# Kernel tuning notes

Measured on AMD Instinct MI355X. Metric: run time of the kernel, lower is better.

The kernel has to match this reference:

```python
import jax, jax.numpy as jnp
import numpy as np

N = 100000   # nodes
E = 1000000  # directed edges
C = 64       # channels
K = 4        # propagation hops
DT = 1.0     # dt; exp_init=False branch: 2*x + dt^2*conv(x) - x_pre


def setup_inputs() -> dict:
    key = jax.random.key(0)
    k1, k2, k3, k4, k5 = jax.random.split(key, 5)
    x = jax.random.normal(k1, (N, C), dtype=jnp.float32)
    x_pre = jax.random.normal(k2, (N, C), dtype=jnp.float32)
    edge_index = jax.random.randint(k3, (2, E), 0, N, dtype=jnp.int32)
    bound = 1.0 / np.sqrt(C)  # PyG Linear default (kaiming-uniform-like)
    W = jax.random.uniform(k4, (C, C), jnp.float32, -bound, bound)
    b = jax.random.uniform(k5, (C,), jnp.float32, -bound, bound)
    return {"x": x, "x_pre": x_pre, "edge_index": edge_index, "W": W, "b": b}


def _sgc(x, edge_index, W, b):
    # gcn_norm: add self-loops, symmetric normalization D^-1/2 (A+I) D^-1/2
    loop = jnp.arange(N, dtype=edge_index.dtype)
    src = jnp.concatenate([edge_index[0], loop])  # source j
    dst = jnp.concatenate([edge_index[1], loop])  # target i
    deg = jax.ops.segment_sum(jnp.ones(src.shape, jnp.float32), dst, num_segments=N)
    dinv = jnp.where(deg > 0, jax.lax.rsqrt(deg), 0.0)
    norm = dinv[src] * dinv[dst]  # [E+N]
    h = x
    for _ in range(K):  # K-hop sparse propagation (gather -> scale -> scatter-add)
        h = jax.ops.segment_sum(h[src] * norm[:, None], dst, num_segments=N)
    return h @ W.T + b  # SGConv final linear


def reference(x, x_pre, edge_index, W, b):
    return 2.0 * x + (DT * DT) * _sgc(x, edge_index, W, b) - x_pre
```

## Files before the change

### kernel.cpp

```cpp
#include <hip/hip_runtime.h>
#include <hip/hip_fp16.h>

#define CCH 64
#define NBLK 128
#define BKT  256


__global__ void countA(const int* __restrict__ dst, int* __restrict__ cntmat,
                       int E, int chunk, int B) {
    __shared__ int h[512];
    int t = threadIdx.x, blk = blockIdx.x;
    for (int i = t; i < B; i += 256) h[i] = 0;
    __syncthreads();
    int e0 = blk * chunk, e1 = min(e0 + chunk, E);
    for (int e = e0 + t; e < e1; e += 256) atomicAdd(&h[dst[e] >> 8], 1);
    __syncthreads();
    for (int i = t; i < B; i += 256) cntmat[i * NBLK + blk] = h[i];
}

__global__ void scan1(const int* __restrict__ cnt, int* __restrict__ part,
                      int* __restrict__ bsum, int N) {
    __shared__ int s[256];
    int t = threadIdx.x;
    int base = blockIdx.x * 1024 + t * 4;
    int v0 = (base + 0 < N) ? cnt[base + 0] : 0;
    int v1 = (base + 1 < N) ? cnt[base + 1] : 0;
    int v2 = (base + 2 < N) ? cnt[base + 2] : 0;
    int v3 = (base + 3 < N) ? cnt[base + 3] : 0;
    s[t] = v0 + v1 + v2 + v3;
    __syncthreads();
    for (int off = 1; off < 256; off <<= 1) {
        int xx = (t >= off) ? s[t - off] : 0;
        __syncthreads();
        s[t] += xx;
        __syncthreads();
    }
    int excl = (t == 0) ? 0 : s[t - 1];
    if (t == 255) bsum[blockIdx.x] = s[255];
    if (base + 0 < N) part[base + 0] = excl;
    if (base + 1 < N) part[base + 1] = excl + v0;
    if (base + 2 < N) part[base + 2] = excl + v0 + v1;
    if (base + 3 < N) part[base + 3] = excl + v0 + v1 + v2;
}

__device__ __forceinline__ void scan_bsum(const int* __restrict__ bsum, int NB2,
                                          int* sbs, int t) {
    int v = (t < NB2) ? bsum[t] : 0;
    sbs[t] = v;
    __syncthreads();
    for (int o = 1; o < 256; o <<= 1) {
        int xx = (t >= o) ? sbs[t - o] : 0;
        __syncthreads();
        sbs[t] += xx;
        __syncthreads();
    }
    int e = sbs[t] - v;
    __syncthreads();
    sbs[t] = e;
    __syncthreads();
}

__global__ void partA(const int* __restrict__ src, const int* __restrict__ dst,
                      const int* __restrict__ part, const int* __restrict__ bsum,
                      unsigned* __restrict__ brec, int E, int chunk, int B, int NB2) {
    __shared__ int cur[512];
    __shared__ int sbs[256];
    int t = threadIdx.x, blk = blockIdx.x;
    scan_bsum(bsum, NB2, sbs, t);
    for (int i = t; i < B; i += 256) {
        int idx = i * NBLK + blk;
        cur[i] = part[idx] + sbs[idx >> 10];
    }
    __syncthreads();
    int e0 = blk * chunk, e1 = min(e0 + chunk, E);
    for (int e = e0 + t; e < e1; e += 256) {
        int s = src[e], d = dst[e];
        int pos = atomicAdd(&cur[d >> 8], 1);
        brec[pos] = ((unsigned)s << 8) | (unsigned)(d & 255);
    }
}

__global__ void buildB(const unsigned* __restrict__ brec, const int* __restrict__ part,
                       const int* __restrict__ bsum, int* __restrict__ row_ptr,
                       int* __restrict__ adj, float* __restrict__ dinv,
                       float* __restrict__ dinv2, const float* __restrict__ x,
                       __half* __restrict__ xh, int N, int B, int E, int NB2) {
    __shared__ int hist[256];
    __shared__ int scanbuf[256];
    __shared__ int cursor[256];
    __shared__ int sbs[256];
    __shared__ float sdinv[256];
    int t = threadIdx.x, k = blockIdx.x;
    scan_bsum(bsum, NB2, sbs, t);
    int i0 = k * NBLK;
    int base = part[i0] + sbs[i0 >> 10];
    int nextb;
    if (k + 1 < B) {
        int i1 = (k + 1) * NBLK;
        nextb = part[i1] + sbs[i1 >> 10];
    } else {
        nextb = E;
    }
    hist[t] = 0;
    __syncthreads();
    for (int i = base + t; i < nextb; i += 256) atomicAdd(&hist[brec[i] & 255u], 1);
    __syncthreads();
    int v = hist[t];
    scanbuf[t] = v;
    __syncthreads();
    for (int o = 1; o < 256; o <<= 1) {
        int xx = (t >= o) ? scanbuf[t - o] : 0;
        __syncthreads();
        scanbuf[t] += xx;
        __syncthreads();
    }
    int excl = scanbuf[t] - v;
    int node = k * 256 + t;
    float di = 0.f;
    if (node < N) {
        int p = base + excl;
        row_ptr[node] = p;
        cursor[t] = p;
        float dp1 = (float)v + 1.0f;
        di = rsqrtf(dp1);
        dinv[node]  = di;
        dinv2[node] = 1.0f / dp1;
    }
    sdinv[t] = di;
    if (k == 0 && t == 0) row_ptr[N] = E;
    __syncthreads();
    for (int i = base + t; i < nextb; i += 256) {
        unsigned r = brec[i];
        int pos = atomicAdd(&cursor[r & 255u], 1);
        adj[pos] = (int)(r >> 8);
    }
    int nodeBase = k * 256;
    for (int i = t; i < 2048; i += 256) {
        int nl = i >> 3;
        int node2 = nodeBase + nl;
        if (node2 < N) {
            float d = sdinv[nl];
            size_t baseE = (size_t)node2 * 64 + (size_t)(i & 7) * 8;
            float4 a = *(const float4*)&x[baseE];
            float4 c = *(const float4*)&x[baseE + 4];
            float4 o;
            __half2* op = (__half2*)&o;
            op[0] = __float22half2_rn(make_float2(d * a.x, d * a.y));
            op[1] = __float22half2_rn(make_float2(d * a.z, d * a.w));
            op[2] = __float22half2_rn(make_float2(d * c.x, d * c.y));
            op[3] = __float22half2_rn(make_float2(d * c.z, d * c.w));
            *(float4*)&xh[baseE] = o;
        }
    }
}


__device__ __forceinline__ void acc16w(float4 hv, float w, float* acc) {
    __half2* hp = (__half2*)&hv;
    #pragma unroll
    for (int i2 = 0; i2 < 4; ++i2) {
        float2 f = __half22float2(hp[i2]);
        acc[2 * i2]     = fmaf(w, f.x, acc[2 * i2]);
        acc[2 * i2 + 1] = fmaf(w, f.y, acc[2 * i2 + 1]);
    }
}

__device__ __forceinline__ void prop_body(const __half* __restrict__ hin,
                                          const int* __restrict__ row_ptr,
                                          const int* __restrict__ adj,
                                          int nodeC, int cnt, int g8, int q,
                                          int E, float* acc) {
    int rp0 = row_ptr[nodeC];

    int R = cnt;
    R = max(R, __shfl_xor(R, 8, 64));
    R = max(R, __shfl_xor(R, 16, 64));
    R = max(R, __shfl_xor(R, 32, 64));

    const float4* hin16 = (const float4*)hin;
    float4 selfv = hin16[(size_t)nodeC * 8 + q];

    int eCur = adj[rp0 + q];
    int eNxt = adj[rp0 + 8 + q];
    int j0 = __shfl(eCur, g8 + 0, 64); j0 = (0 < cnt) ? j0 : 0;
    int j1 = __shfl(eCur, g8 + 1, 64); j1 = (1 < cnt) ? j1 : 0;
    int j2 = __shfl(eCur, g8 + 2, 64); j2 = (2 < cnt) ? j2 : 0;
    int j3 = __shfl(eCur, g8 + 3, 64); j3 = (3 < cnt) ? j3 : 0;
    float4 gA0 = hin16[(size_t)j0 * 8 + q];
    float4 gA1 = hin16[(size_t)j1 * 8 + q];
    float4 gA2 = hin16[(size_t)j2 * 8 + q];
    float4 gA3 = hin16[(size_t)j3 * 8 + q];
    float4 gB0, gB1, gB2, gB3;

    acc16w(selfv, 1.f, acc);

    for (int r = 0; r < R; r += 8) {
        int t;
        t = r + 4; j0 = __shfl(eCur, g8 + (t & 7), 64); j0 = (t < cnt) ? j0 : 0;
        t = r + 5; j1 = __shfl(eCur, g8 + (t & 7), 64); j1 = (t < cnt) ? j1 : 0;
        t = r + 6; j2 = __shfl(eCur, g8 + (t & 7), 64); j2 = (t < cnt) ? j2 : 0;
        t = r + 7; j3 = __shfl(eCur, g8 + (t & 7), 64); j3 = (t < cnt) ? j3 : 0;
        gB0 = hin16[(size_t)j0 * 8 + q];
        gB1 = hin16[(size_t)j1 * 8 + q];
        gB2 = hin16[(size_t)j2 * 8 + q];
        gB3 = hin16[(size_t)j3 * 8 + q];
        float w;
        w = (r + 0 < cnt) ? 1.f : 0.f; acc16w(gA0, w, acc);
        w = (r + 1 < cnt) ? 1.f : 0.f; acc16w(gA1, w, acc);
        w = (r + 2 < cnt) ? 1.f : 0.f; acc16w(gA2, w, acc);
        w = (r + 3 < cnt) ? 1.f : 0.f; acc16w(gA3, w, acc);
        t = r + 8;  j0 = __shfl(eNxt, g8 + (t & 7), 64); j0 = (t < cnt) ? j0 : 0;
        t = r + 9;  j1 = __shfl(eNxt, g8 + (t & 7), 64); j1 = (t < cnt) ? j1 : 0;
        t = r + 10; j2 = __shfl(eNxt, g8 + (t & 7), 64); j2 = (t < cnt) ? j2 : 0;
        t = r + 11; j3 = __shfl(eNxt, g8 + (t & 7), 64); j3 = (t < cnt) ? j3 : 0;
        gA0 = hin16[(size_t)j0 * 8 + q];
        gA1 = hin16[(size_t)j1 * 8 + q];
        gA2 = hin16[(size_t)j2 * 8 + q];
        gA3 = hin16[(size_t)j3 * 8 + q];
        w = (r + 4 < cnt) ? 1.f : 0.f; acc16w(gB0, w, acc);
        w = (r + 5 < cnt) ? 1.f : 0.f; acc16w(gB1, w, acc);
        w = (r + 6 < cnt) ? 1.f : 0.f; acc16w(gB2, w, acc);
        w = (r + 7 < cnt) ? 1.f : 0.f; acc16w(gB3, w, acc);
        eCur = eNxt;
        int ao = rp0 + r + 16;
        ao = (ao > E + 96) ? (E + 96) : ao;
        eNxt = adj[ao + q];
    }
}

__global__ void __launch_bounds__(256, 8)
prop_kernel(const __half* __restrict__ hin, __half* __restrict__ hout,
            const int* __restrict__ row_ptr, const int* __restrict__ adj,
            const float* __restrict__ scale, int N, int E) {
    int wid  = (blockIdx.x * blockDim.x + threadIdx.x) >> 6;
    int lane = threadIdx.x & 63;
    int g    = lane >> 3;
    int q    = lane & 7;
    int nb   = wid << 3;
    if (nb >= N) return;
    int  node  = nb + g;
    bool valid = node < N;
    int  nodeC = valid ? node : (N - 1);
    int cnt = valid ? (row_ptr[nodeC + 1] - row_ptr[nodeC]) : 0;

    float acc[8] = {0.f, 0.f, 0.f, 0.f, 0.f, 0.f, 0.f, 0.f};
    prop_body(hin, row_ptr, adj, nodeC, cnt, g << 3, q, E, acc);

    if (valid) {
        float sc = scale[nodeC];
        float4 o;
        __half2* op = (__half2*)&o;
        op[0] = __float22half2_rn(make_float2(sc * acc[0], sc * acc[1]));
        op[1] = __float22half2_rn(make_float2(sc * acc[2], sc * acc[3]));
        op[2] = __float22half2_rn(make_float2(sc * acc[4], sc * acc[5]));
        op[3] = __float22half2_rn(make_float2(sc * acc[6], sc * acc[7]));
        ((float4*)hout)[(size_t)node * 8 + q] = o;
    }
}

__global__ void __launch_bounds__(256, 6)
prop_final_kernel(const __half* __restrict__ hin, const float* __restrict__ x,
                  const float* __restrict__ xp, const float* __restrict__ W,
                  const float* __restrict__ b, float* __restrict__ out,
                  const int* __restrict__ row_ptr, const int* __restrict__ adj,
                  const float* __restrict__ dinv, int N, int E) {
    __shared__ __align__(16) float Wt[64 * 68];
    __shared__ __align__(16) float ht[32 * 68];
    int t = threadIdx.x;
    int nodeBase = blockIdx.x * 32;

    for (int i = t; i < 1024; i += 256) {
        int c  = i >> 4;
        int k4 = i & 15;
        float4 w4 = ((const float4*)W)[i];
        Wt[(k4 * 4 + 0) * 68 + c] = w4.x;
        Wt[(k4 * 4 + 1) * 68 + c] = w4.y;
        Wt[(k4 * 4 + 2) * 68 + c] = w4.z;
        Wt[(k4 * 4 + 3) * 68 + c] = w4.w;
    }

    int wv   = t >> 6;
    int lane = t & 63;
    int g    = lane >> 3;
    int q    = lane & 7;
    int nl   = wv * 8 + g;
    int node = nodeBase + nl;
    bool valid = node < N;
    int  nodeC = valid ? node : (N - 1);
    int cnt = valid ? (row_ptr[nodeC + 1] - row_ptr[nodeC]) : 0;

    float acc[8] = {0.f, 0.f, 0.f, 0.f, 0.f, 0.f, 0.f, 0.f};
    prop_body(hin, row_ptr, adj, nodeC, cnt, g << 3, q, E, acc);

    float sc = valid ? dinv[nodeC] : 0.f;
    {
        float* hrow = &ht[nl * 68 + q * 8];
        float4 h0, h1;
        h0.x = sc * acc[0]; h0.y = sc * acc[1]; h0.z = sc * acc[2]; h0.w = sc * acc[3];
        h1.x = sc * acc[4]; h1.y = sc * acc[5]; h1.z = sc * acc[6]; h1.w = sc * acc[7];
        *(float4*)&hrow[0] = h0;
        *(float4*)&hrow[4] = h1;
    }

    int r0 = t >> 4;
    int c0 = (t & 15) * 4;
    int n0 = nodeBase + r0;
    int n1 = n0 + 16;
    int n0c = (n0 < N) ? n0 : (N - 1);
    int n1c = (n1 < N) ? n1 : (N - 1);
    float4 xv0 = *(const float4*)&x[n0c * 64 + c0];
    float4 pv0 = *(const float4*)&xp[n0c * 64 + c0];
    float4 xv1 = *(const float4*)&x[n1c * 64 + c0];
    float4 pv1 = *(const float4*)&xp[n1c * 64 + c0];
    float4 bv  = *(const float4*)&b[c0];

    __syncthreads();

    float4 av0 = make_float4(0.f, 0.f, 0.f, 0.f);
    float4 av1 = make_float4(0.f, 0.f, 0.f, 0.f);
    #pragma unroll 4
    for (int k4 = 0; k4 < 16; ++k4) {
        float4 w0 = *(const float4*)&Wt[(k4 * 4 + 0) * 68 + c0];
        float4 w1 = *(const float4*)&Wt[(k4 * 4 + 1) * 68 + c0];
        float4 w2 = *(const float4*)&Wt[(k4 * 4 + 2) * 68 + c0];
        float4 w3 = *(const float4*)&Wt[(k4 * 4 + 3) * 68 + c0];
        float4 ha = *(const float4*)&ht[r0 * 68 + k4 * 4];
        float4 hb = *(const float4*)&ht[(r0 + 16) * 68 + k4 * 4];
        av0.x = fmaf(ha.x, w0.x, av0.x); av0.y = fmaf(ha.x, w0.y, av0.y);
        av0.z = fmaf(ha.x, w0.z, av0.z); av0.w = fmaf(ha.x, w0.w, av0.w);
        av0.x = fmaf(ha.y, w1.x, av0.x); av0.y = fmaf(ha.y, w1.y, av0.y);
        av0.z = fmaf(ha.y, w1.z, av0.z); av0.w = fmaf(ha.y, w1.w, av0.w);
        av0.x = fmaf(ha.z, w2.x, av0.x); av0.y = fmaf(ha.z, w2.y, av0.y);
        av0.z = fmaf(ha.z, w2.z, av0.z); av0.w = fmaf(ha.z, w2.w, av0.w);
        av0.x = fmaf(ha.w, w3.x, av0.x); av0.y = fmaf(ha.w, w3.y, av0.y);
        av0.z = fmaf(ha.w, w3.z, av0.z); av0.w = fmaf(ha.w, w3.w, av0.w);
        av1.x = fmaf(hb.x, w0.x, av1.x); av1.y = fmaf(hb.x, w0.y, av1.y);
        av1.z = fmaf(hb.x, w0.z, av1.z); av1.w = fmaf(hb.x, w0.w, av1.w);
        av1.x = fmaf(hb.y, w1.x, av1.x); av1.y = fmaf(hb.y, w1.y, av1.y);
        av1.z = fmaf(hb.y, w1.z, av1.z); av1.w = fmaf(hb.y, w1.w, av1.w);
        av1.x = fmaf(hb.z, w2.x, av1.x); av1.y = fmaf(hb.z, w2.y, av1.y);
        av1.z = fmaf(hb.z, w2.z, av1.z); av1.w = fmaf(hb.z, w2.w, av1.w);
        av1.x = fmaf(hb.w, w3.x, av1.x); av1.y = fmaf(hb.w, w3.y, av1.y);
        av1.z = fmaf(hb.w, w3.z, av1.z); av1.w = fmaf(hb.w, w3.w, av1.w);
    }

    if (n0 < N) {
        int base = n0 * 64 + c0;
        float4 o;
        o.x = fmaf(2.f, xv0.x, av0.x + bv.x) - pv0.x;
        o.y = fmaf(2.f, xv0.y, av0.y + bv.y) - pv0.y;
        o.z = fmaf(2.f, xv0.z, av0.z + bv.z) - pv0.z;
        o.w = fmaf(2.f, xv0.w, av0.w + bv.w) - pv0.w;
        *(float4*)&out[base] = o;
    }
    if (n1 < N) {
        int base = n1 * 64 + c0;
        float4 o;
        o.x = fmaf(2.f, xv1.x, av1.x + bv.x) - pv1.x;
        o.y = fmaf(2.f, xv1.y, av1.y + bv.y) - pv1.y;
        o.z = fmaf(2.f, xv1.z, av1.z + bv.z) - pv1.z;
        o.w = fmaf(2.f, xv1.w, av1.w + bv.w) - pv1.w;
        *(float4*)&out[base] = o;
    }
}

extern "C" void kernel_launch(void* const* d_in, const int* in_sizes, int n_in,
                              void* d_out, int out_size, void* d_ws, size_t ws_size,
                              hipStream_t stream) {
    const float* x    = (const float*)d_in[0];
    const float* xpre = (const float*)d_in[1];
    const int*   ei   = (const int*)d_in[2];
    const float* W    = (const float*)d_in[3];
    const float* b    = (const float*)d_in[4];
    float* out = (float*)d_out;

    const int N = in_sizes[0] / CCH;
    const int E = in_sizes[2] / 2;
    const int* src = ei;
    const int* dst = ei + E;

    const int B     = (N + BKT - 1) / BKT;
    const int M     = B * NBLK;
    const int chunk = (E + NBLK - 1) / NBLK;
    const int NB2   = (M + 1023) / 1024;

    char* p = (char*)d_ws;
    auto alloc = [&](size_t bytes) -> char* {
        char* r = p;
        p += (bytes + 255) & ~(size_t)255;
        return r;
    };
    int*      cntmat  = (int*)alloc((size_t)M * 4);
    int*      part    = (int*)alloc((size_t)M * 4);
    int*      bsum    = (int*)alloc((size_t)NB2 * 4);
    unsigned* brec    = (unsigned*)alloc((size_t)E * 4);
    int*      adj     = (int*)alloc(((size_t)E + 128) * 4);
    int*      row_ptr = (int*)alloc(((size_t)N + 1) * 4);
    float*    dinv    = (float*)alloc((size_t)N * 4);
    float*    dinv2   = (float*)alloc((size_t)N * 4);
    __half*   xh      = (__half*)alloc((size_t)N * CCH * 2);
    __half*   g0      = (__half*)alloc((size_t)N * CCH * 2);
    __half*   g1      = (__half*)alloc((size_t)N * CCH * 2);

    countA<<<NBLK, 256, 0, stream>>>(dst, cntmat, E, chunk, B);
    scan1 <<<NB2, 256, 0, stream>>>(cntmat, part, bsum, M);
    partA <<<NBLK, 256, 0, stream>>>(src, dst, part, bsum, brec, E, chunk, B, NB2);
    buildB<<<B, 256, 0, stream>>>(brec, part, bsum, row_ptr, adj, dinv, dinv2,
                                  x, xh, N, B, E, NB2);

    const int nwave = (N + 7) / 8;
    const int pgrid = (nwave + 3) / 4;
    prop_kernel<<<pgrid, 256, 0, stream>>>(xh, g0, row_ptr, adj, dinv2, N, E);
    prop_kernel<<<pgrid, 256, 0, stream>>>(g0, g1, row_ptr, adj, dinv2, N, E);
    prop_kernel<<<pgrid, 256, 0, stream>>>(g1, g0, row_ptr, adj, dinv2, N, E);
    prop_final_kernel<<<(N + 31) / 32, 256, 0, stream>>>(g0, x, xpre, W, b, out,
                                                         row_ptr, adj, dinv, N, E);
    (void)g1;
}
```

Measured before the change: 245.1 us.

## Sort nodes by degree within buckets to balance per-wave gather work

buildB now counting-sorts the nodes of each 256-node bucket by in-degree and writes a permutation array. All propagation kernels index nodes through this permutation, so the eight nodes sharing a wave have similar degree and less lane divergence in the unrolled gather loop. The final kernel also loads W into shared memory with scalar transposed reads instead of float4 scatter. The cost is an extra indirection per node, a few more scans in buildB, and scattered output rows instead of contiguous ones.

```diff
diff --git a/kernel.cpp b/kernel.cpp
--- a/kernel.cpp
+++ b/kernel.cpp
@@ -84,11 +84,13 @@
                        const int* __restrict__ bsum, int* __restrict__ row_ptr,
                        int* __restrict__ adj, float* __restrict__ dinv,
                        float* __restrict__ dinv2, const float* __restrict__ x,
-                       __half* __restrict__ xh, int N, int B, int E, int NB2) {
+                       __half* __restrict__ xh, int* __restrict__ perm,
+                       int N, int B, int E, int NB2) {
     __shared__ int hist[256];
     __shared__ int scanbuf[256];
     __shared__ int cursor[256];
     __shared__ int sbs[256];
+    __shared__ int dh[256];
     __shared__ float sdinv[256];
     int t = threadIdx.x, k = blockIdx.x;
     scan_bsum(bsum, NB2, sbs, t);
@@ -102,6 +104,7 @@
         nextb = E;
     }
     hist[t] = 0;
+    dh[t] = 0;
     __syncthreads();
     for (int i = base + t; i < nextb; i += 256) atomicAdd(&hist[brec[i] & 255u], 1);
     __syncthreads();
@@ -117,6 +120,7 @@
     int excl = scanbuf[t] - v;
     int node = k * 256 + t;
     float di = 0.f;
+    int d = 255;
     if (node < N) {
         int p = base + excl;
         row_ptr[node] = p;
@@ -125,30 +129,48 @@
         di = rsqrtf(dp1);
         dinv[node]  = di;
         dinv2[node] = 1.0f / dp1;
+        d = (v < 255) ? v : 254;
     }
     sdinv[t] = di;
     if (k == 0 && t == 0) row_ptr[N] = E;
+    atomicAdd(&dh[d], 1);
     __syncthreads();
     for (int i = base + t; i < nextb; i += 256) {
         unsigned r = brec[i];
         int pos = atomicAdd(&cursor[r & 255u], 1);
         adj[pos] = (int)(r >> 8);
+    }
+    __syncthreads();
+    int dv = dh[t];
+    scanbuf[t] = dv;
+    __syncthreads();
+    for (int o = 1; o < 256; o <<= 1) {
+        int xx = (t >= o) ? scanbuf[t - o] : 0;
+        __syncthreads();
+        scanbuf[t] += xx;
+        __syncthreads();
+    }
+    hist[t] = scanbuf[t] - dv;
+    __syncthreads();
+    if (node < N) {
+        int r = atomicAdd(&hist[d], 1);
+        perm[k * 256 + r] = node;
     }
     int nodeBase = k * 256;
     for (int i = t; i < 2048; i += 256) {
         int nl = i >> 3;
         int node2 = nodeBase + nl;
         if (node2 < N) {
-            float d = sdinv[nl];
+            float dsc = sdinv[nl];
             size_t baseE = (size_t)node2 * 64 + (size_t)(i & 7) * 8;
             float4 a = *(const float4*)&x[baseE];
             float4 c = *(const float4*)&x[baseE + 4];
             float4 o;
             __half2* op = (__half2*)&o;
-            op[0] = __float22half2_rn(make_float2(d * a.x, d * a.y));
-            op[1] = __float22half2_rn(make_float2(d * a.z, d * a.w));
-            op[2] = __float22half2_rn(make_float2(d * c.x, d * c.y));
-            op[3] = __float22half2_rn(make_float2(d * c.z, d * c.w));
+            op[0] = __float22half2_rn(make_float2(dsc * a.x, dsc * a.y));
+            op[1] = __float22half2_rn(make_float2(dsc * a.z, dsc * a.w));
+            op[2] = __float22half2_rn(make_float2(dsc * c.x, dsc * c.y));
+            op[3] = __float22half2_rn(make_float2(dsc * c.z, dsc * c.w));
             *(float4*)&xh[baseE] = o;
         }
     }
@@ -231,23 +253,24 @@
 __global__ void __launch_bounds__(256, 8)
 prop_kernel(const __half* __restrict__ hin, __half* __restrict__ hout,
             const int* __restrict__ row_ptr, const int* __restrict__ adj,
-            const float* __restrict__ scale, int N, int E) {
+            const float* __restrict__ scale, const int* __restrict__ perm,
+            int N, int E) {
     int wid  = (blockIdx.x * blockDim.x + threadIdx.x) >> 6;
     int lane = threadIdx.x & 63;
     int g    = lane >> 3;
     int q    = lane & 7;
     int nb   = wid << 3;
     if (nb >= N) return;
-    int  node  = nb + g;
-    bool valid = node < N;
-    int  nodeC = valid ? node : (N - 1);
-    int cnt = valid ? (row_ptr[nodeC + 1] - row_ptr[nodeC]) : 0;
+    int  slot  = nb + g;
+    bool valid = slot < N;
+    int  node  = perm[valid ? slot : (N - 1)];
+    int cnt = valid ? (row_ptr[node + 1] - row_ptr[node]) : 0;
 
     float acc[8] = {0.f, 0.f, 0.f, 0.f, 0.f, 0.f, 0.f, 0.f};
-    prop_body(hin, row_ptr, adj, nodeC, cnt, g << 3, q, E, acc);
+    prop_body(hin, row_ptr, adj, node, cnt, g << 3, q, E, acc);
 
     if (valid) {
-        float sc = scale[nodeC];
+        float sc = scale[node];
         float4 o;
         __half2* op = (__half2*)&o;
         op[0] = __float22half2_rn(make_float2(sc * acc[0], sc * acc[1]));
@@ -263,20 +286,21 @@
                   const float* __restrict__ xp, const float* __restrict__ W,
                   const float* __restrict__ b, float* __restrict__ out,
                   const int* __restrict__ row_ptr, const int* __restrict__ adj,
-                  const float* __restrict__ dinv, int N, int E) {
+                  const float* __restrict__ dinv, const int* __restrict__ perm,
+                  int N, int E) {
     __shared__ __align__(16) float Wt[64 * 68];
     __shared__ __align__(16) float ht[32 * 68];
     int t = threadIdx.x;
     int nodeBase = blockIdx.x * 32;
 
-    for (int i = t; i < 1024; i += 256) {
-        int c  = i >> 4;
-        int k4 = i & 15;
-        float4 w4 = ((const float4*)W)[i];
-        Wt[(k4 * 4 + 0) * 68 + c] = w4.x;
-        Wt[(k4 * 4 + 1) * 68 + c] = w4.y;
-        Wt[(k4 * 4 + 2) * 68 + c] = w4.z;
-        Wt[(k4 * 4 + 3) * 68 + c] = w4.w;
+    {
+        int kr = t >> 6;
+        int c  = t & 63;
+        #pragma unroll
+        for (int it = 0; it < 16; ++it) {
+            int kk = it * 4 + kr;
+            Wt[kk * 68 + c] = W[c * 64 + kk];
+        }
     }
 
     int wv   = t >> 6;
@@ -284,15 +308,15 @@
     int g    = lane >> 3;
     int q    = lane & 7;
     int nl   = wv * 8 + g;
-    int node = nodeBase + nl;
-    bool valid = node < N;
-    int  nodeC = valid ? node : (N - 1);
-    int cnt = valid ? (row_ptr[nodeC + 1] - row_ptr[nodeC]) : 0;
+    int slot = nodeBase + nl;
+    bool valid = slot < N;
+    int  node  = perm[valid ? slot : (N - 1)];
+    int cnt = valid ? (row_ptr[node + 1] - row_ptr[node]) : 0;
 
     float acc[8] = {0.f, 0.f, 0.f, 0.f, 0.f, 0.f, 0.f, 0.f};
-    prop_body(hin, row_ptr, adj, nodeC, cnt, g << 3, q, E, acc);
-
-    float sc = valid ? dinv[nodeC] : 0.f;
+    prop_body(hin, row_ptr, adj, node, cnt, g << 3, q, E, acc);
+
+    float sc = valid ? dinv[node] : 0.f;
     {
         float* hrow = &ht[nl * 68 + q * 8];
         float4 h0, h1;
@@ -304,14 +328,14 @@
 
     int r0 = t >> 4;
     int c0 = (t & 15) * 4;
-    int n0 = nodeBase + r0;
-    int n1 = n0 + 16;
-    int n0c = (n0 < N) ? n0 : (N - 1);
-    int n1c = (n1 < N) ? n1 : (N - 1);
-    float4 xv0 = *(const float4*)&x[n0c * 64 + c0];
-    float4 pv0 = *(const float4*)&xp[n0c * 64 + c0];
-    float4 xv1 = *(const float4*)&x[n1c * 64 + c0];
-    float4 pv1 = *(const float4*)&xp[n1c * 64 + c0];
+    int s0 = nodeBase + r0;
+    int s1 = s0 + 16;
+    int n0 = perm[(s0 < N) ? s0 : (N - 1)];
+    int n1 = perm[(s1 < N) ? s1 : (N - 1)];
+    float4 xv0 = *(const float4*)&x[n0 * 64 + c0];
+    float4 pv0 = *(const float4*)&xp[n0 * 64 + c0];
+    float4 xv1 = *(const float4*)&x[n1 * 64 + c0];
+    float4 pv1 = *(const float4*)&xp[n1 * 64 + c0];
     float4 bv  = *(const float4*)&b[c0];
 
     __syncthreads();
@@ -344,7 +368,7 @@
         av1.z = fmaf(hb.w, w3.z, av1.z); av1.w = fmaf(hb.w, w3.w, av1.w);
     }
 
-    if (n0 < N) {
+    if (s0 < N) {
         int base = n0 * 64 + c0;
         float4 o;
         o.x = fmaf(2.f, xv0.x, av0.x + bv.x) - pv0.x;
@@ -353,7 +377,7 @@
         o.w = fmaf(2.f, xv0.w, av0.w + bv.w) - pv0.w;
         *(float4*)&out[base] = o;
     }
-    if (n1 < N) {
+    if (s1 < N) {
         int base = n1 * 64 + c0;
         float4 o;
         o.x = fmaf(2.f, xv1.x, av1.x + bv.x) - pv1.x;
@@ -398,6 +422,7 @@
     int*      row_ptr = (int*)alloc(((size_t)N + 1) * 4);
     float*    dinv    = (float*)alloc((size_t)N * 4);
     float*    dinv2   = (float*)alloc((size_t)N * 4);
+    int*      perm    = (int*)alloc((size_t)N * 4);
     __half*   xh      = (__half*)alloc((size_t)N * CCH * 2);
     __half*   g0      = (__half*)alloc((size_t)N * CCH * 2);
     __half*   g1      = (__half*)alloc((size_t)N * CCH * 2);
@@ -406,14 +431,15 @@
     scan1 <<<NB2, 256, 0, stream>>>(cntmat, part, bsum, M);
     partA <<<NBLK, 256, 0, stream>>>(src, dst, part, bsum, brec, E, chunk, B, NB2);
     buildB<<<B, 256, 0, stream>>>(brec, part, bsum, row_ptr, adj, dinv, dinv2,
-                                  x, xh, N, B, E, NB2);
+                                  x, xh, perm, N, B, E, NB2);
 
     const int nwave = (N + 7) / 8;
     const int pgrid = (nwave + 3) / 4;
-    prop_kernel<<<pgrid, 256, 0, stream>>>(xh, g0, row_ptr, adj, dinv2, N, E);
-    prop_kernel<<<pgrid, 256, 0, stream>>>(g0, g1, row_ptr, adj, dinv2, N, E);
-    prop_kernel<<<pgrid, 256, 0, stream>>>(g1, g0, row_ptr, adj, dinv2, N, E);
+    prop_kernel<<<pgrid, 256, 0, stream>>>(xh, g0, row_ptr, adj, dinv2, perm, N, E);
+    prop_kernel<<<pgrid, 256, 0, stream>>>(g0, g1, row_ptr, adj, dinv2, perm, N, E);
+    prop_kernel<<<pgrid, 256, 0, stream>>>(g1, g0, row_ptr, adj, dinv2, perm, N, E);
     prop_final_kernel<<<(N + 31) / 32, 256, 0, stream>>>(g0, x, xpre, W, b, out,
-                                                         row_ptr, adj, dinv, N, E);
+                                                         row_ptr, adj, dinv, perm,
+                                                         N, E);
     (void)g1;
 }
```

Result: slower. 278.0 us (+13.4%).

## Raise partition block count and split degree/fp16 conversion into separate kernel

Applied to the files above, without the earlier changes.

Increases the number of blocks used for edge counting and partitioning from 128 to 512 to better fill the GPU. Degree is now computed with global atomics during counting, and a new dedicated kernel computes dinv and the scaled fp16 copy of x, removing that work from buildB. This adds a memset, an extra launch and a million global atomics in exchange for more parallelism in the preprocessing stages.

```diff
diff --git a/kernel.cpp b/kernel.cpp
--- a/kernel.cpp
+++ b/kernel.cpp
@@ -2,18 +2,22 @@
 #include <hip/hip_fp16.h>
 
 #define CCH 64
-#define NBLK 128
+#define NBLK 512
 #define BKT  256
 
 
 __global__ void countA(const int* __restrict__ dst, int* __restrict__ cntmat,
-                       int E, int chunk, int B) {
+                       int* __restrict__ deg, int E, int chunk, int B) {
     __shared__ int h[512];
     int t = threadIdx.x, blk = blockIdx.x;
     for (int i = t; i < B; i += 256) h[i] = 0;
     __syncthreads();
     int e0 = blk * chunk, e1 = min(e0 + chunk, E);
-    for (int e = e0 + t; e < e1; e += 256) atomicAdd(&h[dst[e] >> 8], 1);
+    for (int e = e0 + t; e < e1; e += 256) {
+        int d = dst[e];
+        atomicAdd(&h[d >> 8], 1);
+        atomicAdd(&deg[d], 1);
+    }
     __syncthreads();
     for (int i = t; i < B; i += 256) cntmat[i * NBLK + blk] = h[i];
 }
@@ -80,16 +84,36 @@
     }
 }
 
+__global__ void __launch_bounds__(256, 8)
+tohalfK(const int* __restrict__ deg, const float* __restrict__ x,
+        float* __restrict__ dinv, float* __restrict__ dinv2,
+        __half* __restrict__ xh, int N) {
+    int t = threadIdx.x;
+    int node = blockIdx.x * 32 + (t >> 3);
+    if (node >= N) return;
+    int q = t & 7;
+    float dp1 = (float)deg[node] + 1.0f;
+    float di = rsqrtf(dp1);
+    if (q == 0) { dinv[node] = di; dinv2[node] = 1.0f / dp1; }
+    size_t base = (size_t)node * 64 + (size_t)q * 8;
+    float4 a = *(const float4*)&x[base];
+    float4 c = *(const float4*)&x[base + 4];
+    float4 o;
+    __half2* op = (__half2*)&o;
+    op[0] = __float22half2_rn(make_float2(di * a.x, di * a.y));
+    op[1] = __float22half2_rn(make_float2(di * a.z, di * a.w));
+    op[2] = __float22half2_rn(make_float2(di * c.x, di * c.y));
+    op[3] = __float22half2_rn(make_float2(di * c.z, di * c.w));
+    *(float4*)&xh[base] = o;
+}
+
 __global__ void buildB(const unsigned* __restrict__ brec, const int* __restrict__ part,
                        const int* __restrict__ bsum, int* __restrict__ row_ptr,
-                       int* __restrict__ adj, float* __restrict__ dinv,
-                       float* __restrict__ dinv2, const float* __restrict__ x,
-                       __half* __restrict__ xh, int N, int B, int E, int NB2) {
+                       int* __restrict__ adj, int N, int B, int E, int NB2) {
     __shared__ int hist[256];
     __shared__ int scanbuf[256];
     __shared__ int cursor[256];
     __shared__ int sbs[256];
-    __shared__ float sdinv[256];
     int t = threadIdx.x, k = blockIdx.x;
     scan_bsum(bsum, NB2, sbs, t);
     int i0 = k * NBLK;
@@ -116,41 +140,17 @@
     }
     int excl = scanbuf[t] - v;
     int node = k * 256 + t;
-    float di = 0.f;
     if (node < N) {
         int p = base + excl;
         row_ptr[node] = p;
         cursor[t] = p;
-        float dp1 = (float)v + 1.0f;
-        di = rsqrtf(dp1);
-        dinv[node]  = di;
-        dinv2[node] = 1.0f / dp1;
-    }
-    sdinv[t] = di;
+    }
     if (k == 0 && t == 0) row_ptr[N] = E;
     __syncthreads();
     for (int i = base + t; i < nextb; i += 256) {
         unsigned r = brec[i];
         int pos = atomicAdd(&cursor[r & 255u], 1);
         adj[pos] = (int)(r >> 8);
-    }
-    int nodeBase = k * 256;
-    for (int i = t; i < 2048; i += 256) {
-        int nl = i >> 3;
-        int node2 = nodeBase + nl;
-        if (node2 < N) {
-            float d = sdinv[nl];
-            size_t baseE = (size_t)node2 * 64 + (size_t)(i & 7) * 8;
-            float4 a = *(const float4*)&x[baseE];
-            float4 c = *(const float4*)&x[baseE + 4];
-            float4 o;
-            __half2* op = (__half2*)&o;
-            op[0] = __float22half2_rn(make_float2(d * a.x, d * a.y));
-            op[1] = __float22half2_rn(make_float2(d * a.z, d * a.w));
-            op[2] = __float22half2_rn(make_float2(d * c.x, d * c.y));
-            op[3] = __float22half2_rn(make_float2(d * c.z, d * c.w));
-            *(float4*)&xh[baseE] = o;
-        }
     }
 }
 
@@ -396,17 +396,19 @@
     unsigned* brec    = (unsigned*)alloc((size_t)E * 4);
     int*      adj     = (int*)alloc(((size_t)E + 128) * 4);
     int*      row_ptr = (int*)alloc(((size_t)N + 1) * 4);
+    int*      deg     = (int*)alloc((size_t)N * 4);
     float*    dinv    = (float*)alloc((size_t)N * 4);
     float*    dinv2   = (float*)alloc((size_t)N * 4);
     __half*   xh      = (__half*)alloc((size_t)N * CCH * 2);
     __half*   g0      = (__half*)alloc((size_t)N * CCH * 2);
     __half*   g1      = (__half*)alloc((size_t)N * CCH * 2);
 
-    countA<<<NBLK, 256, 0, stream>>>(dst, cntmat, E, chunk, B);
+    hipMemsetAsync(deg, 0, (size_t)N * 4, stream);
+    countA<<<NBLK, 256, 0, stream>>>(dst, cntmat, deg, E, chunk, B);
     scan1 <<<NB2, 256, 0, stream>>>(cntmat, part, bsum, M);
     partA <<<NBLK, 256, 0, stream>>>(src, dst, part, bsum, brec, E, chunk, B, NB2);
-    buildB<<<B, 256, 0, stream>>>(brec, part, bsum, row_ptr, adj, dinv, dinv2,
-                                  x, xh, N, B, E, NB2);
+    tohalfK<<<(N + 31) / 32, 256, 0, stream>>>(deg, x, dinv, dinv2, xh, N);
+    buildB<<<B, 256, 0, stream>>>(brec, part, bsum, row_ptr, adj, N, B, E, NB2);
 
     const int nwave = (N + 7) / 8;
     const int pgrid = (nwave + 3) / 4;
```

Result: slower. 275.8 us (+12.5%).
